# Optimization experiments

Hardware: AMD Instinct MI355X
Metric: run time of the kernel (lower is better)

## Reference

```python
import jax, jax.numpy as jnp
import numpy as np

B, L, D, H, OUT = 4, 2048, 1024, 8, 256
DH = D // H
EPS = 1e-12


def setup_inputs() -> dict:
    key = jax.random.key(0)
    ks = jax.random.split(key, 20)
    s = lambda fan_in: 1.0 / np.sqrt(fan_in)
    def lin(k, fin, fout):
        k1, k2 = jax.random.split(k)
        w = jax.random.uniform(k1, (fin, fout), jnp.float32, -s(fin), s(fin))
        b = jax.random.uniform(k2, (fout,), jnp.float32, -s(fin), s(fin))
        return w, b
    x = jax.random.normal(ks[0], (B, L, D), jnp.float32)
    wq, bq = lin(ks[1], D, D)
    wk, bk = lin(ks[2], D, D)
    wv, bv = lin(ks[3], D, D)
    gamma = jnp.ones((D,), jnp.float32)
    beta = jnp.zeros((D,), jnp.float32)
    wff, bff = lin(ks[4], D, D)
    wc1, bc1 = lin(ks[5], D, D)
    wc2, bc2 = lin(ks[6], D, 1)
    wl1, bl1 = lin(ks[7], L, L)
    wl2, bl2 = lin(ks[8], L, OUT)
    return dict(x=x, wq=wq, bq=bq, wk=wk, bk=bk, wv=wv, bv=bv,
                gamma=gamma, beta=beta, wff=wff, bff=bff,
                wc1=wc1, bc1=bc1, wc2=wc2, bc2=bc2,
                wl1=wl1, bl1=bl1, wl2=wl2, bl2=bl2)


def layernorm(x, gamma, beta):
    mean = x.mean(-1, keepdims=True)
    var = ((x - mean) ** 2).mean(-1, keepdims=True)  # biased variance
    return gamma * (x - mean) / jnp.sqrt(var + EPS) + beta


def reference(x, wq, bq, wk, bk, wv, bv, gamma, beta, wff, bff,
              wc1, bc1, wc2, bc2, wl1, bl1, wl2, bl2):
    # multi-head self-attention (dropout = identity at inference)
    q = (x @ wq + bq).reshape(B, L, H, DH)
    k = (x @ wk + bk).reshape(B, L, H, DH)
    v = (x @ wv + bv).reshape(B, L, H, DH)
    scores = jnp.einsum('bqhd,bkhd->bhqk', q, k) / np.sqrt(DH)
    attn = jax.nn.softmax(scores, axis=-1)                  # [B,H,L,L]
    ctx = jnp.einsum('bhqk,bkhd->bqhd', attn, v).reshape(B, L, D)
    h = layernorm(x + ctx, gamma, beta)
    # feedforward: Linear + ReLU (hidden = d_model), residual + same layernorm params
    ff = jax.nn.relu(h @ wff + bff)
    h = layernorm(h + ff, gamma, beta)
    # collapse d_model -> 1
    c = jax.nn.relu(h @ wc1 + bc1)
    c = jax.nn.relu(c @ wc2 + bc2)                          # [B,L,1]
    c = jnp.squeeze(c, axis=-1)                             # [B,L]
    # collapse length -> out_featuresize
    c = jax.nn.relu(c @ wl1 + bl1)
    out = c @ wl2 + bl2                                     # [B,OUT]
    return out
```

## Files before the change

### kernel.cpp

```cpp
#include <hip/hip_runtime.h>

typedef unsigned short u16;
typedef unsigned int u32;
typedef __attribute__((ext_vector_type(4))) float f32x4;
typedef __attribute__((ext_vector_type(8))) short short8;
typedef __attribute__((ext_vector_type(4))) u32 u32x4;
typedef __attribute__((ext_vector_type(4))) u16 u16x4;

#define BB 4
#define LL 2048
#define DD 1024
#define HH 8
#define DHH 128

__device__ __forceinline__ u16 f2b(float f) {
  u32 u = __builtin_bit_cast(u32, f);
  u += 0x7fffu + ((u >> 16) & 1u);
  return (u16)(u >> 16);
}
__device__ __forceinline__ float b2f(u16 h) {
  u32 u = ((u32)h) << 16;
  return __builtin_bit_cast(float, u);
}
__device__ __forceinline__ float exp2_fast(float x) {
  float r;
  asm("v_exp_f32 %0, %1" : "=v"(r) : "v"(x));
  return r;
}
__device__ __forceinline__ u32 packbf(float a, float b) {
  return (u32)f2b(a) | ((u32)f2b(b) << 16);
}
__device__ __forceinline__ u32 bperm(int srcLane, u32 v) {
  return (u32)__builtin_amdgcn_ds_bpermute(srcLane << 2, (int)v);
}

#define GLDS16(g, l)                                                          \
  __builtin_amdgcn_global_load_lds(                                           \
      (const __attribute__((address_space(1))) void*)(g),                     \
      (__attribute__((address_space(3))) void*)(l), 16, 0, 0)

__global__ __launch_bounds__(256) void cvt_k(const float* __restrict__ X,
                                             u16* __restrict__ Xb, long n) {
  long i = ((long)blockIdx.x * 256 + threadIdx.x) * 4;
  if (i >= n) return;
  f32x4 v = *(const f32x4*)(X + i);
  u16x4 o;
#pragma unroll
  for (int k = 0; k < 4; k++) o[k] = f2b(v[k]);
  *(u16x4*)(Xb + i) = o;
}

__global__ __launch_bounds__(256) void tr_k(const float* __restrict__ W,
                                            u16* __restrict__ WT) {
  __shared__ float tile[32][33];
  const int bx = blockIdx.x, by = blockIdx.y;
  const int tx = threadIdx.x & 31, ty = threadIdx.x >> 5;
#pragma unroll
  for (int i = 0; i < 4; i++)
    tile[ty + i * 8][tx] =
        W[(long)(by * 32 + ty + i * 8) * 1024 + bx * 32 + tx];
  __syncthreads();
#pragma unroll
  for (int i = 0; i < 4; i++)
    WT[(long)(bx * 32 + ty + i * 8) * 1024 + by * 32 + tx] =
        f2b(tile[tx][ty + i * 8]);
}

template <bool RELU, int OMODE>
__global__ __launch_bounds__(256, 2) void gemm_k(
    const u16* __restrict__ A, const u16* __restrict__ BT,
    const float* __restrict__ bias, float scale, float* __restrict__ Cf,
    u16* __restrict__ Cb, int M, int N, int K) {
  __shared__ u16 As[2][128 * 32];
  __shared__ u16 Bs[2][128 * 32];
  const int nwg = gridDim.x * gridDim.y;
  const int bid = blockIdx.x + blockIdx.y * gridDim.x;
  const int swz = (bid & 7) * (nwg >> 3) + (bid >> 3);
  const int bxi = swz % gridDim.x, byi = swz / gridDim.x;
  const int t = threadIdx.x;
  const int l = t & 63, w = t >> 6;
  const int lr = l & 15, lg = l >> 4;
  const int wr = (w >> 1) * 64, wc = (w & 1) * 64;
  const long bm = (long)byi * 128, bn = (long)bxi * 128;
  const int srow = l >> 2;
  const int scol = (l & 3) * 8;
  const u16* Ag0 = A + (bm + w * 32 + srow) * (long)K + scol;
  const u16* Ag1 = A + (bm + w * 32 + 16 + srow) * (long)K + scol;
  const u16* Bg0 = BT + (bn + w * 32 + srow) * (long)K + scol;
  const u16* Bg1 = BT + (bn + w * 32 + 16 + srow) * (long)K + scol;
  const int wo = w * 1024;
  f32x4 acc[4][4] = {};
  GLDS16(Ag0, &As[0][wo]);
  GLDS16(Ag1, &As[0][wo + 512]);
  GLDS16(Bg0, &Bs[0][wo]);
  GLDS16(Bg1, &Bs[0][wo + 512]);
  __syncthreads();
  int cur = 0;
  for (int k0 = 0; k0 < K; k0 += 32) {
    const int nxt = cur ^ 1;
    if (k0 + 32 < K) {
      GLDS16(Ag0 + k0 + 32, &As[nxt][wo]);
      GLDS16(Ag1 + k0 + 32, &As[nxt][wo + 512]);
      GLDS16(Bg0 + k0 + 32, &Bs[nxt][wo]);
      GLDS16(Bg1 + k0 + 32, &Bs[nxt][wo + 512]);
    }
    short8 af[4], bf[4];
#pragma unroll
    for (int i = 0; i < 4; i++)
      af[i] = *(const short8*)&As[cur][(wr + i * 16 + lr) * 32 + lg * 8];
#pragma unroll
    for (int i = 0; i < 4; i++)
      bf[i] = *(const short8*)&Bs[cur][(wc + i * 16 + lr) * 32 + lg * 8];
#pragma unroll
    for (int i = 0; i < 4; i++)
#pragma unroll
      for (int j = 0; j < 4; j++)
        acc[i][j] = __builtin_amdgcn_mfma_f32_16x16x32_bf16(af[i], bf[j],
                                                            acc[i][j], 0, 0, 0);
    __syncthreads();
    cur = nxt;
  }
#pragma unroll
  for (int i = 0; i < 4; i++)
#pragma unroll
    for (int j = 0; j < 4; j++) {
      long col = bn + wc + j * 16 + lr;
      float bv = bias[col];
      if (OMODE == 2) {
        long row0 = bm + wr + i * 16 + lg * 4;
        long b = row0 >> 11, l0 = row0 & 2047;
        u16x4 ov;
#pragma unroll
        for (int r = 0; r < 4; r++) {
          float v2 = (acc[i][j][r] + bv) * scale;
          if (RELU) v2 = fmaxf(v2, 0.f);
          ov[r] = f2b(v2);
        }
        *(u16x4*)(Cb + (b * 1024 + col) * 2048 + l0) = ov;
      } else {
#pragma unroll
        for (int r = 0; r < 4; r++) {
          long row = bm + wr + i * 16 + lg * 4 + r;
          float v2 = (acc[i][j][r] + bv) * scale;
          if (RELU) v2 = fmaxf(v2, 0.f);
          if (OMODE == 1)
            Cb[row * N + col] = f2b(v2);
          else
            Cf[row * N + col] = v2;
        }
      }
    }
}

__global__ __launch_bounds__(512, 4) void flash_k(const u16* __restrict__ Q,
                                                  const u16* __restrict__ Kb,
                                                  const u16* __restrict__ VT,
                                                  float* __restrict__ ctx) {
  __shared__ u16 Ks[2][64][136];
  __shared__ u16 VTs[2][128][72];
  const int nwg = gridDim.x * gridDim.y;
  const int bid = blockIdx.x + blockIdx.y * gridDim.x;
  const int swz = (bid & 7) * (nwg >> 3) + (bid >> 3);
  const int bxi = swz % gridDim.x, byi = swz / gridDim.x;
  const int t = threadIdx.x;
  const int l = t & 63, w = t >> 6;
  const int lr = l & 15, lg = l >> 4;
  const int b = byi >> 3, h = byi & 7;
  const long kbase = ((long)b * LL) * DD + h * DHH;
  const long vtbase = ((long)(b * 8 + h) * DHH) * LL;
  const int q0 = bxi * 128;

  short8 qf[4];
  {
    const u16* qp = Q + kbase + (long)(q0 + w * 16 + lr) * DD + lg * 8;
#pragma unroll
    for (int c = 0; c < 4; c++) qf[c] = *(const short8*)(qp + c * 32);
  }
  f32x4 oacc[8] = {};
  float mprev = -1e30f;
  float lsum = 0.f;

  const int krow = t >> 3, kcol = (t & 7) * 16;
  const int vrow = t >> 2, vcol = (t & 3) * 16;
  u32x4 kr0, kr1, vr0, vr1;
  {
    const u16* kp = Kb + kbase + (long)krow * DD + kcol;
    kr0 = *(const u32x4*)(kp);
    kr1 = *(const u32x4*)(kp + 8);
    const u16* vp = VT + vtbase + (long)vrow * LL + vcol;
    vr0 = *(const u32x4*)(vp);
    vr1 = *(const u32x4*)(vp + 8);
    *(u32x4*)&Ks[0][krow][kcol] = kr0;
    *(u32x4*)&Ks[0][krow][kcol + 8] = kr1;
    *(u32x4*)&VTs[0][vrow][vcol] = vr0;
    *(u32x4*)&VTs[0][vrow][vcol + 8] = vr1;
  }
  const int NT = LL / 64;
  for (int it = 0; it < NT; ++it) {
    const int cur = it & 1;
    if (it + 1 < NT) {
      const u16* kp = Kb + kbase + (long)((it + 1) * 64 + krow) * DD + kcol;
      kr0 = *(const u32x4*)(kp);
      kr1 = *(const u32x4*)(kp + 8);
      const u16* vp = VT + vtbase + (long)vrow * LL + (it + 1) * 64 + vcol;
      vr0 = *(const u32x4*)(vp);
      vr1 = *(const u32x4*)(vp + 8);
    }
    __syncthreads();

    f32x4 s[4] = {};
#pragma unroll
    for (int jc = 0; jc < 4; jc++)
#pragma unroll
      for (int c = 0; c < 4; c++) {
        short8 kf = *(const short8*)&Ks[cur][jc * 16 + lr][c * 32 + lg * 8];
        s[jc] =
            __builtin_amdgcn_mfma_f32_16x16x32_bf16(kf, qf[c], s[jc], 0, 0, 0);
      }

    float mx = fmaxf(fmaxf(s[0][0], s[0][1]), fmaxf(s[0][2], s[0][3]));
#pragma unroll
    for (int jc = 1; jc < 4; jc++)
      mx = fmaxf(mx, fmaxf(fmaxf(s[jc][0], s[jc][1]),
                           fmaxf(s[jc][2], s[jc][3])));
    mx = fmaxf(mx, __shfl_xor(mx, 16, 64));
    mx = fmaxf(mx, __shfl_xor(mx, 32, 64));

    if (__any((int)(mx > mprev + 8.f))) {
      float mn = fmaxf(mprev, mx);
      float alpha = exp2_fast(mprev - mn);
      mprev = mn;
      lsum *= alpha;
      float ar[4];
#pragma unroll
      for (int r = 0; r < 4; r++) ar[r] = __shfl(alpha, lg * 4 + r, 64);
#pragma unroll
      for (int d8 = 0; d8 < 8; d8++)
#pragma unroll
        for (int r = 0; r < 4; r++) oacc[d8][r] *= ar[r];
    }

    u32 pk2[4][2];
    float ladd = 0.f;
#pragma unroll
    for (int jc = 0; jc < 4; jc++) {
      float p0 = exp2_fast(s[jc][0] - mprev);
      float p1 = exp2_fast(s[jc][1] - mprev);
      float p2 = exp2_fast(s[jc][2] - mprev);
      float p3 = exp2_fast(s[jc][3] - mprev);
      ladd += (p0 + p1) + (p2 + p3);
      pk2[jc][0] = packbf(p0, p1);
      pk2[jc][1] = packbf(p2, p3);
    }
    lsum += ladd;

    short8 pf[2];
#pragma unroll
    for (int kk = 0; kk < 2; kk++) {
      u32x4 afv;
#pragma unroll
      for (int m = 0; m < 4; m++) {
        int srcl = lr + ((((lg & 1) << 1) + (m >> 1)) << 4);
        u32 a0 = bperm(srcl, pk2[2 * kk][m & 1]);
        u32 a1 = bperm(srcl, pk2[2 * kk + 1][m & 1]);
        afv[m] = (lg >> 1) ? a1 : a0;
      }
      pf[kk] = __builtin_bit_cast(short8, afv);
    }

#pragma unroll
    for (int kk = 0; kk < 2; kk++)
#pragma unroll
      for (int d8 = 0; d8 < 8; d8++) {
        short8 vf = *(const short8*)&VTs[cur][d8 * 16 + lr][kk * 32 + lg * 8];
        oacc[d8] =
            __builtin_amdgcn_mfma_f32_16x16x32_bf16(pf[kk], vf, oacc[d8], 0,
                                                    0, 0);
      }

    if (it + 1 < NT) {
      *(u32x4*)&Ks[cur ^ 1][krow][kcol] = kr0;
      *(u32x4*)&Ks[cur ^ 1][krow][kcol + 8] = kr1;
      *(u32x4*)&VTs[cur ^ 1][vrow][vcol] = vr0;
      *(u32x4*)&VTs[cur ^ 1][vrow][vcol + 8] = vr1;
    }
  }

  lsum += __shfl_xor(lsum, 16, 64);
  lsum += __shfl_xor(lsum, 32, 64);
#pragma unroll
  for (int r = 0; r < 4; r++) {
    float inv = 1.f / __shfl(lsum, lg * 4 + r, 64);
    float* cp = ctx + kbase + (long)(q0 + w * 16 + lg * 4 + r) * DD;
#pragma unroll
    for (int d8 = 0; d8 < 8; d8++) cp[d8 * 16 + lr] = oacc[d8][r] * inv;
  }
}

__global__ __launch_bounds__(256) void ln_k(const float* __restrict__ X,
                                            const float* __restrict__ R,
                                            const float* __restrict__ gamma,
                                            const float* __restrict__ beta,
                                            float* __restrict__ Hf,
                                            u16* __restrict__ Hb) {
  const int row = blockIdx.x, t = threadIdx.x;
  const long off = (long)row * DD + t * 4;
  f32x4 v = *(const f32x4*)(X + off);
  f32x4 rv = *(const f32x4*)(R + off);
#pragma unroll
  for (int i = 0; i < 4; i++) v[i] += rv[i];
  float s = v[0] + v[1] + v[2] + v[3];
  float q = v[0] * v[0] + v[1] * v[1] + v[2] * v[2] + v[3] * v[3];
#pragma unroll
  for (int m = 32; m >= 1; m >>= 1) {
    s += __shfl_xor(s, m, 64);
    q += __shfl_xor(q, m, 64);
  }
  __shared__ float red[8];
  if ((t & 63) == 0) {
    red[t >> 6] = s;
    red[4 + (t >> 6)] = q;
  }
  __syncthreads();
  s = red[0] + red[1] + red[2] + red[3];
  q = red[4] + red[5] + red[6] + red[7];
  const float mean = s * (1.f / 1024.f);
  const float var = q * (1.f / 1024.f) - mean * mean;
  const float rstd = rsqrtf(var + 1e-12f);
  f32x4 g = *(const f32x4*)(gamma + t * 4);
  f32x4 be = *(const f32x4*)(beta + t * 4);
  f32x4 o;
#pragma unroll
  for (int i = 0; i < 4; i++) o[i] = g[i] * (v[i] - mean) * rstd + be[i];
  if (Hf) *(f32x4*)(Hf + off) = o;
  if (Hb) {
    u16x4 ob;
#pragma unroll
    for (int i = 0; i < 4; i++) ob[i] = f2b(o[i]);
    *(u16x4*)(Hb + off) = ob;
  }
}

__global__ __launch_bounds__(256) void c2_k(const u16* __restrict__ C,
                                            const float* __restrict__ wc2,
                                            const float* __restrict__ bc2,
                                            float* __restrict__ cvec) {
  const int row = blockIdx.x, t = threadIdx.x;
  u16x4 cv = *(const u16x4*)(C + (long)row * DD + t * 4);
  f32x4 wv = *(const f32x4*)(wc2 + t * 4);
  float s = b2f(cv[0]) * wv[0] + b2f(cv[1]) * wv[1] + b2f(cv[2]) * wv[2] +
            b2f(cv[3]) * wv[3];
#pragma unroll
  for (int m = 32; m >= 1; m >>= 1) s += __shfl_xor(s, m, 64);
  __shared__ float red[4];
  if ((t & 63) == 0) red[t >> 6] = s;
  __syncthreads();
  if (t == 0)
    cvec[row] = fmaxf(red[0] + red[1] + red[2] + red[3] + bc2[0], 0.f);
}

__global__ __launch_bounds__(256) void smm_part(const float* __restrict__ Cin,
                                                const float* __restrict__ W,
                                                float* __restrict__ P, int Lr,
                                                int N, int SL) {
  const int j = blockIdx.x * 256 + threadIdx.x;
  const int l0 = blockIdx.y * SL;
  float a0 = 0, a1 = 0, a2 = 0, a3 = 0;
  for (int ll = l0; ll < l0 + SL; ll++) {
    float wv = W[(long)ll * N + j];
    a0 += Cin[ll] * wv;
    a1 += Cin[Lr + ll] * wv;
    a2 += Cin[2 * Lr + ll] * wv;
    a3 += Cin[3 * Lr + ll] * wv;
  }
  float* Pp = P + ((long)blockIdx.y * 4) * N + j;
  Pp[0] = a0;
  Pp[N] = a1;
  Pp[2 * N] = a2;
  Pp[3 * N] = a3;
}

template <bool RELU>
__global__ __launch_bounds__(256) void smm_red(const float* __restrict__ P,
                                               const float* __restrict__ bias,
                                               float* __restrict__ Out, int N,
                                               int S) {
  const int j = blockIdx.x * 256 + threadIdx.x;
#pragma unroll
  for (int b = 0; b < 4; b++) {
    float a = 0;
    for (int s = 0; s < S; s++) a += P[((long)s * 4 + b) * N + j];
    a += bias[j];
    if (RELU) a = fmaxf(a, 0.f);
    Out[(long)b * N + j] = a;
  }
}

extern "C" void kernel_launch(void* const* d_in, const int* in_sizes, int n_in,
                              void* d_out, int out_size, void* d_ws,
                              size_t ws_size, hipStream_t stream) {
  (void)in_sizes; (void)n_in; (void)out_size; (void)ws_size;
  const float* x = (const float*)d_in[0];
  const float* wq = (const float*)d_in[1];
  const float* bq = (const float*)d_in[2];
  const float* wk = (const float*)d_in[3];
  const float* bk = (const float*)d_in[4];
  const float* wv = (const float*)d_in[5];
  const float* bv = (const float*)d_in[6];
  const float* gamma = (const float*)d_in[7];
  const float* beta = (const float*)d_in[8];
  const float* wff = (const float*)d_in[9];
  const float* bff = (const float*)d_in[10];
  const float* wc1 = (const float*)d_in[11];
  const float* bc1 = (const float*)d_in[12];
  const float* wc2 = (const float*)d_in[13];
  const float* bc2 = (const float*)d_in[14];
  const float* wl1 = (const float*)d_in[15];
  const float* bl1 = (const float*)d_in[16];
  const float* wl2 = (const float*)d_in[17];
  const float* bl2 = (const float*)d_in[18];

  char* wsp = (char*)d_ws;
  size_t off = 0;
  auto take = [&](size_t bytes) -> char* {
    char* p = wsp + off;
    off += (bytes + 255) & ~(size_t)255;
    return p;
  };
  u16* xb = (u16*)take((size_t)8192 * 1024 * 2);
  u16* wqT = (u16*)take((size_t)1024 * 1024 * 2);
  u16* wkT = (u16*)take((size_t)1024 * 1024 * 2);
  u16* wvT = (u16*)take((size_t)1024 * 1024 * 2);
  u16* wffT = (u16*)take((size_t)1024 * 1024 * 2);
  u16* wc1T = (u16*)take((size_t)1024 * 1024 * 2);
  u16* qb = (u16*)take((size_t)8192 * 1024 * 2);
  u16* kbuf = (u16*)take((size_t)8192 * 1024 * 2);
  u16* vT = (u16*)take((size_t)8192 * 1024 * 2);
  float* ctxb = (float*)take((size_t)8192 * 1024 * 4);
  float* h1f = (float*)take((size_t)8192 * 1024 * 4);
  float* cvec = (float*)take(8192 * 4);
  float* c3 = (float*)take(8192 * 4);
  float* P1 = (float*)take((size_t)16 * 4 * 2048 * 4);
  float* P2 = (float*)take((size_t)16 * 4 * 256 * 4);
  u16* h1b = qb;
  u16* h2b = kbuf;
  u16* cb = vT;
  float* ff = ctxb;

  cvt_k<<<8192, 256, 0, stream>>>(x, xb, (long)8192 * 1024);
  dim3 trg(32, 32);
  tr_k<<<trg, 256, 0, stream>>>(wq, wqT);
  tr_k<<<trg, 256, 0, stream>>>(wk, wkT);
  tr_k<<<trg, 256, 0, stream>>>(wv, wvT);
  tr_k<<<trg, 256, 0, stream>>>(wff, wffT);
  tr_k<<<trg, 256, 0, stream>>>(wc1, wc1T);

  dim3 gg(8, 64);
  gemm_k<false, 1><<<gg, 256, 0, stream>>>(
      xb, wqT, bq, 0.12751743f, nullptr, qb, 8192, 1024, 1024);
  gemm_k<false, 1><<<gg, 256, 0, stream>>>(xb, wkT, bk, 1.f, nullptr, kbuf,
                                           8192, 1024, 1024);
  gemm_k<false, 2><<<gg, 256, 0, stream>>>(xb, wvT, bv, 1.f, nullptr, vT,
                                           8192, 1024, 1024);
  flash_k<<<dim3(16, 32), 512, 0, stream>>>(qb, kbuf, vT, ctxb);
  ln_k<<<8192, 256, 0, stream>>>(x, ctxb, gamma, beta, h1f, h1b);
  gemm_k<true, 0><<<gg, 256, 0, stream>>>(h1b, wffT, bff, 1.f, ff, nullptr,
                                          8192, 1024, 1024);
  ln_k<<<8192, 256, 0, stream>>>(h1f, ff, gamma, beta, nullptr, h2b);
  gemm_k<true, 1><<<gg, 256, 0, stream>>>(h2b, wc1T, bc1, 1.f, nullptr, cb,
                                          8192, 1024, 1024);
  c2_k<<<8192, 256, 0, stream>>>(cb, wc2, bc2, cvec);
  smm_part<<<dim3(8, 16), 256, 0, stream>>>(cvec, wl1, P1, 2048, 2048, 128);
  smm_red<true><<<8, 256, 0, stream>>>(P1, bl1, c3, 2048, 16);
  smm_part<<<dim3(1, 16), 256, 0, stream>>>(c3, wl2, P2, 2048, 256, 128);
  smm_red<false><<<1, 256, 0, stream>>>(P2, bl2, (float*)d_out, 256, 16);
}
```

Baseline: 402.1 us.

## Load flash-attention K/V tiles directly into LDS with XOR-swizzled layout

The flash attention kernel now fills its double-buffered K and V^T shared-memory tiles with direct global-to-LDS 16-byte loads (GLDS16). Before, each tile was staged through registers and written to shared memory after the MFMA work. Row padding, previously used to avoid bank conflicts, is replaced by an XOR swizzle of 8-element column groups, applied on both the global source address and the fragment read address. The barrier moves to the end of each iteration, so the prefetch into the other buffer overlaps the current tile's compute. This is meant to cut register pressure and the VGPR-to-LDS store instructions, but it depends on the async loads being complete at the barrier and on the swizzle indices being correct.

```diff
diff --git a/kernel.cpp b/kernel.cpp
--- a/kernel.cpp
+++ b/kernel.cpp
@@ -156,8 +156,8 @@
                                                   const u16* __restrict__ Kb,
                                                   const u16* __restrict__ VT,
                                                   float* __restrict__ ctx) {
-  __shared__ u16 Ks[2][64][136];
-  __shared__ u16 VTs[2][128][72];
+  __shared__ u16 Ks2[2][64 * 128];
+  __shared__ u16 Vs2[2][128 * 64];
   const int nwg = gridDim.x * gridDim.y;
   const int bid = blockIdx.x + blockIdx.y * gridDim.x;
   const int swz = (bid & 7) * (nwg >> 3) + (bid >> 3);
@@ -180,40 +180,56 @@
   float mprev = -1e30f;
   float lsum = 0.f;
 
-  const int krow = t >> 3, kcol = (t & 7) * 16;
-  const int vrow = t >> 2, vcol = (t & 3) * 16;
-  u32x4 kr0, kr1, vr0, vr1;
-  {
-    const u16* kp = Kb + kbase + (long)krow * DD + kcol;
-    kr0 = *(const u32x4*)(kp);
-    kr1 = *(const u32x4*)(kp + 8);
-    const u16* vp = VT + vtbase + (long)vrow * LL + vcol;
-    vr0 = *(const u32x4*)(vp);
-    vr1 = *(const u32x4*)(vp + 8);
-    *(u32x4*)&Ks[0][krow][kcol] = kr0;
-    *(u32x4*)&Ks[0][krow][kcol + 8] = kr1;
-    *(u32x4*)&VTs[0][vrow][vcol] = vr0;
-    *(u32x4*)&VTs[0][vrow][vcol + 8] = vr1;
-  }
+  const int krA = w * 8 + (l >> 4);
+  const int krB = krA + 4;
+  const int kc16 = l & 15;
+  const int vrA = w * 16 + (l >> 3);
+  const int vrB = vrA + 8;
+  const int vc16 = l & 7;
+  const u16* kg0 = Kb + kbase + (long)krA * DD + (kc16 ^ (krA & 7)) * 8;
+  const u16* kg1 = Kb + kbase + (long)krB * DD + (kc16 ^ (krB & 7)) * 8;
+  const u16* vg0 = VT + vtbase + (long)vrA * LL + (vc16 ^ (vrA & 7)) * 8;
+  const u16* vg1 = VT + vtbase + (long)vrB * LL + (vc16 ^ (vrB & 7)) * 8;
+  u16* const kl0 = &Ks2[0][(w * 8) * 128];
+  u16* const kl1 = &Ks2[0][(w * 8 + 4) * 128];
+  u16* const vl0 = &Vs2[0][(w * 16) * 64];
+  u16* const vl1 = &Vs2[0][(w * 16 + 8) * 64];
+  GLDS16(kg0, kl0);
+  GLDS16(kg1, kl1);
+  GLDS16(vg0, vl0);
+  GLDS16(vg1, vl1);
+  __syncthreads();
+
+  int colk[4], colv[2];
+#pragma unroll
+  for (int c = 0; c < 4; c++) colk[c] = (((c * 4 + lg) ^ (lr & 7)) * 8);
+#pragma unroll
+  for (int kk = 0; kk < 2; kk++) colv[kk] = (((kk * 4 + lg) ^ (lr & 7)) * 8);
+
   const int NT = LL / 64;
   for (int it = 0; it < NT; ++it) {
     const int cur = it & 1;
     if (it + 1 < NT) {
-      const u16* kp = Kb + kbase + (long)((it + 1) * 64 + krow) * DD + kcol;
-      kr0 = *(const u32x4*)(kp);
-      kr1 = *(const u32x4*)(kp + 8);
-      const u16* vp = VT + vtbase + (long)vrow * LL + (it + 1) * 64 + vcol;
-      vr0 = *(const u32x4*)(vp);
-      vr1 = *(const u32x4*)(vp + 8);
-    }
-    __syncthreads();
+      kg0 += 64 * DD;
+      kg1 += 64 * DD;
+      vg0 += 64;
+      vg1 += 64;
+      const int ko = (cur ^ 1) * (64 * 128);
+      const int vo = (cur ^ 1) * (128 * 64);
+      GLDS16(kg0, kl0 + ko);
+      GLDS16(kg1, kl1 + ko);
+      GLDS16(vg0, vl0 + vo);
+      GLDS16(vg1, vl1 + vo);
+    }
+    const u16* Kc = &Ks2[cur][0];
+    const u16* Vc = &Vs2[cur][0];
 
     f32x4 s[4] = {};
 #pragma unroll
     for (int jc = 0; jc < 4; jc++)
 #pragma unroll
       for (int c = 0; c < 4; c++) {
-        short8 kf = *(const short8*)&Ks[cur][jc * 16 + lr][c * 32 + lg * 8];
+        short8 kf = *(const short8*)&Kc[(jc * 16 + lr) * 128 + colk[c]];
         s[jc] =
             __builtin_amdgcn_mfma_f32_16x16x32_bf16(kf, qf[c], s[jc], 0, 0, 0);
       }
@@ -272,18 +288,12 @@
     for (int kk = 0; kk < 2; kk++)
 #pragma unroll
       for (int d8 = 0; d8 < 8; d8++) {
-        short8 vf = *(const short8*)&VTs[cur][d8 * 16 + lr][kk * 32 + lg * 8];
+        short8 vf = *(const short8*)&Vc[(d8 * 16 + lr) * 64 + colv[kk]];
         oacc[d8] =
             __builtin_amdgcn_mfma_f32_16x16x32_bf16(pf[kk], vf, oacc[d8], 0,
                                                     0, 0);
       }
-
-    if (it + 1 < NT) {
-      *(u32x4*)&Ks[cur ^ 1][krow][kcol] = kr0;
-      *(u32x4*)&Ks[cur ^ 1][krow][kcol + 8] = kr1;
-      *(u32x4*)&VTs[cur ^ 1][vrow][vcol] = vr0;
-      *(u32x4*)&VTs[cur ^ 1][vrow][vcol + 8] = vr1;
-    }
+    __syncthreads();
   }
 
   lsum += __shfl_xor(lsum, 16, 64);
```

New measurement: 395.0 us. No clear change (-1.8%).
